# Kernel optimization log

Hardware: AMD Instinct MI355X
Metric: run time of the kernel (lower is better)

The kernel has to match this reference:

```python
import jax, jax.numpy as jnp
import numpy as np

N0, N1, N2 = 200000, 100000, 50000
D = 16          # sampled neighbor fan-out
DIM = 128       # input_dim == hidden dims


def setup_inputs() -> dict:
    key = jax.random.key(0)
    ks = jax.random.split(key, 9)
    return {
        "features": jax.random.normal(ks[0], (N0, DIM), jnp.float32),
        "W1": jax.random.normal(ks[1], (2 * DIM, DIM), jnp.float32) * 0.02,
        "b1": jnp.zeros((DIM,), jnp.float32),
        "W2": jax.random.normal(ks[2], (2 * DIM, DIM), jnp.float32) * 0.02,
        "b2": jnp.zeros((DIM,), jnp.float32),
        "neigh1_idx": jax.random.randint(ks[3], (N1, D), 0, N0, jnp.int32),
        "self1_idx": jax.random.randint(ks[4], (N1,), 0, N0, jnp.int32),
        "neigh2_idx": jax.random.randint(ks[5], (N2, D), 0, N1, jnp.int32),
        "self2_idx": jax.random.randint(ks[6], (N2,), 0, N1, jnp.int32),
    }


def _sage_layer(h_prev, self_idx, neigh_idx, W, b):
    # mean-aggregate sampled neighbors: gather [n, D, d] -> mean over D
    neigh = jnp.mean(h_prev[neigh_idx], axis=1)          # [n, d]
    x = jnp.concatenate([h_prev[self_idx], neigh], axis=-1)  # [n, 2d]
    return jax.nn.relu(x @ W + b)                        # [n, d_out]


def reference(features, W1, b1, W2, b2, neigh1_idx, self1_idx, neigh2_idx, self2_idx):
    h1 = _sage_layer(features, self1_idx, neigh1_idx, W1, b1)  # [N1, DIM]
    h2 = _sage_layer(h1, self2_idx, neigh2_idx, W2, b2)        # [N2, DIM]
    return h2
```

## Files before the change

### kernel.cpp

```cpp
#include <hip/hip_runtime.h>
#include <hip/hip_bf16.h>

typedef __attribute__((ext_vector_type(8))) short bf16x8;
typedef __attribute__((ext_vector_type(4))) float f32x4;

#define DIM   128
#define KD    256
#define FAN   16
#define TILE  32
#define XS_STRIDE 264
#define WP_LAYER_SHORTS (8*8*64*8)

__device__ __forceinline__ unsigned short f2bf(float f) {
    __hip_bfloat16 h = __float2bfloat16(f);
    return *reinterpret_cast<unsigned short*>(&h);
}
__device__ __forceinline__ float bflo(unsigned int u) { return __uint_as_float(u << 16); }
__device__ __forceinline__ float bfhi(unsigned int u) { return __uint_as_float(u & 0xffff0000u); }

__global__ __launch_bounds__(256)
void cvt_bf16_kernel(const float* __restrict__ in, uint2* __restrict__ out, int n4)
{
    const int stride = gridDim.x * blockDim.x;
    for (int i = blockIdx.x * blockDim.x + threadIdx.x; i < n4; i += stride) {
        const float4 v = reinterpret_cast<const float4*>(in)[i];
        uint2 o;
        o.x = (unsigned int)f2bf(v.x) | ((unsigned int)f2bf(v.y) << 16);
        o.y = (unsigned int)f2bf(v.z) | ((unsigned int)f2bf(v.w) << 16);
        out[i] = o;
    }
}

__global__ __launch_bounds__(256)
void wpack_kernel(const float* __restrict__ W1, const float* __restrict__ W2,
                  unsigned short* __restrict__ wp)
{
    const int b = blockIdx.x;
    const float* W = (b & 8) ? W2 : W1;
    unsigned short* dst = wp + ((b & 8) ? WP_LAYER_SHORTS : 0);
    const int t   = b & 7;
    const int tid = threadIdx.x;
    const int lane = tid & 63, wid = tid >> 6;
    const int l15 = lane & 15, lg = lane >> 4;
    #pragma unroll
    for (int s = 0; s < 2; ++s) {
        const int ks = wid + s * 4;
        bf16x8 v;
        #pragma unroll
        for (int j = 0; j < 8; ++j)
            v[j] = (short)f2bf(W[(size_t)(ks * 32 + lg * 8 + j) * DIM + t * 16 + l15]);
        *reinterpret_cast<bf16x8*>(dst + ((size_t)(t * 8 + ks) * 64 + lane) * 8) = v;
    }
}

template<bool SRC_BF, bool DST_BF>
__global__ __launch_bounds__(256, 4)
void sage_layer(const void* __restrict__ src,
                const unsigned short* __restrict__ wp,
                const float* __restrict__ bias,
                const int*  __restrict__ nidx,
                const int*  __restrict__ sidx,
                void* __restrict__ dst,
                int nnodes)
{
    __shared__ unsigned short xs[TILE * XS_STRIDE];

    const int tid  = threadIdx.x;
    const int lane = tid & 63;
    const int wid  = tid >> 6;
    const int l15  = lane & 15;
    const int lg   = lane >> 4;
    const int nb   = blockIdx.x * TILE;

    #pragma unroll 4
    for (int i = 0; i < 8; ++i) {
        int n = nb + wid * 8 + i;
        if (n >= nnodes) n = nnodes - 1;
        const int sn = sidx[n];
        const int* nn = nidx + (size_t)n * FAN;
        unsigned int su;
        float ax = 0.f, ay = 0.f;
        if (SRC_BF) {
            const unsigned int* srcu = (const unsigned int*)src;
            su = srcu[(size_t)sn * 64 + lane];
            #pragma unroll
            for (int j = 0; j < FAN; ++j) {
                const unsigned int u = srcu[(size_t)nn[j] * 64 + lane];
                ax += bflo(u); ay += bfhi(u);
            }
        } else {
            const float* srcf = (const float*)src;
            const float2 sv = *reinterpret_cast<const float2*>(srcf + (size_t)sn * DIM + 2 * lane);
            su = (unsigned int)f2bf(sv.x) | ((unsigned int)f2bf(sv.y) << 16);
            #pragma unroll
            for (int j = 0; j < FAN; ++j) {
                const float2 v = *reinterpret_cast<const float2*>(srcf + (size_t)nn[j] * DIM + 2 * lane);
                ax += v.x; ay += v.y;
            }
        }
        ax *= 0.0625f; ay *= 0.0625f;
        const unsigned int mu = (unsigned int)f2bf(ax) | ((unsigned int)f2bf(ay) << 16);
        unsigned int* row = reinterpret_cast<unsigned int*>(xs + (size_t)(wid * 8 + i) * XS_STRIDE);
        row[lane]      = su;
        row[64 + lane] = mu;
    }

    bf16x8 wf[2][8];
    #pragma unroll
    for (int t = 0; t < 2; ++t) {
        const int tg = 2 * wid + t;
        #pragma unroll
        for (int ks = 0; ks < 8; ++ks)
            wf[t][ks] = *reinterpret_cast<const bf16x8*>(
                wp + ((size_t)(tg * 8 + ks) * 64 + lane) * 8);
    }
    float bv[2];
    bv[0] = bias[(2 * wid + 0) * 16 + l15];
    bv[1] = bias[(2 * wid + 1) * 16 + l15];

    __syncthreads();

    f32x4 acc[2][2];
    #pragma unroll
    for (int mt = 0; mt < 2; ++mt)
        #pragma unroll
        for (int t = 0; t < 2; ++t)
            acc[mt][t] = (f32x4){0.f, 0.f, 0.f, 0.f};

    #pragma unroll
    for (int ks = 0; ks < 8; ++ks) {
        bf16x8 af[2];
        #pragma unroll
        for (int mt = 0; mt < 2; ++mt)
            af[mt] = *reinterpret_cast<const bf16x8*>(
                xs + (size_t)(mt * 16 + l15) * XS_STRIDE + ks * 32 + lg * 8);
        #pragma unroll
        for (int mt = 0; mt < 2; ++mt)
            #pragma unroll
            for (int t = 0; t < 2; ++t)
                acc[mt][t] = __builtin_amdgcn_mfma_f32_16x16x32_bf16(
                    af[mt], wf[t][ks], acc[mt][t], 0, 0, 0);
    }

    #pragma unroll
    for (int mt = 0; mt < 2; ++mt) {
        #pragma unroll
        for (int t = 0; t < 2; ++t) {
            const int col = (2 * wid + t) * 16 + l15;
            #pragma unroll
            for (int r = 0; r < 4; ++r) {
                const int n = nb + mt * 16 + lg * 4 + r;
                if (n < nnodes) {
                    const float v = acc[mt][t][r] + bv[t];
                    const float rv = v > 0.f ? v : 0.f;
                    if (DST_BF)
                        ((unsigned short*)dst)[(size_t)n * DIM + col] = f2bf(rv);
                    else
                        ((float*)dst)[(size_t)n * DIM + col] = rv;
                }
            }
        }
    }
}

extern "C" void kernel_launch(void* const* d_in, const int* in_sizes, int n_in,
                              void* d_out, int out_size, void* d_ws, size_t ws_size,
                              hipStream_t stream)
{
    const float* features = (const float*)d_in[0];
    const float* W1       = (const float*)d_in[1];
    const float* b1       = (const float*)d_in[2];
    const float* W2       = (const float*)d_in[3];
    const float* b2       = (const float*)d_in[4];
    const int*   n1idx    = (const int*)d_in[5];
    const int*   s1idx    = (const int*)d_in[6];
    const int*   n2idx    = (const int*)d_in[7];
    const int*   s2idx    = (const int*)d_in[8];

    const int NF = in_sizes[0];
    const int N1 = in_sizes[6];
    const int N2 = in_sizes[8];

    const size_t fbf_bytes = (size_t)NF * 2;
    const size_t h1_bytes  = (size_t)N1 * DIM * 2;
    const size_t wp_bytes  = (size_t)2 * WP_LAYER_SHORTS * 2;
    const bool full = ws_size >= fbf_bytes + h1_bytes + wp_bytes;

    unsigned char* ws = (unsigned char*)d_ws;
    unsigned short* fbf = nullptr;
    unsigned short* h1  = nullptr;
    unsigned short* wpk = nullptr;
    if (full) {
        fbf = (unsigned short*)ws;
        h1  = (unsigned short*)(ws + fbf_bytes);
        wpk = (unsigned short*)(ws + fbf_bytes + h1_bytes);
    } else {
        h1  = (unsigned short*)ws;
        wpk = (unsigned short*)(ws + h1_bytes);
    }

    wpack_kernel<<<16, 256, 0, stream>>>(W1, W2, wpk);
    if (full)
        cvt_bf16_kernel<<<2048, 256, 0, stream>>>(features, (uint2*)fbf, NF / 4);

    const int t1 = (N1 + TILE - 1) / TILE;
    const int t2 = (N2 + TILE - 1) / TILE;

    if (full)
        sage_layer<true,  true><<<t1, 256, 0, stream>>>(fbf, wpk, b1, n1idx, s1idx, h1, N1);
    else
        sage_layer<false, true><<<t1, 256, 0, stream>>>(features, wpk, b1, n1idx, s1idx, h1, N1);

    sage_layer<true, false><<<t2, 256, 0, stream>>>(h1, wpk + WP_LAYER_SHORTS, b2,
                                                    n2idx, s2idx, (float*)d_out, N2);
}
```

Before: 274.2 us.

## Restructure SAGE layer into single-wave blocks streaming weights from memory

Changes each block to one 64-lane wave handling a 16-node tile, which removes the block barrier and the register-resident weight fragments. Weights are now loaded from global memory per k-step for all 8 output column tiles, and the loop is not unrolled. The aim is lower register and LDS pressure for more resident waves to hide gather latency. The cost is that every block re-reads the full packed weight matrix, adding L2 traffic, and each wave gathers its 16 nodes serially.

```diff
diff --git a/kernel.cpp b/kernel.cpp
--- a/kernel.cpp
+++ b/kernel.cpp
@@ -7,7 +7,7 @@
 #define DIM   128
 #define KD    256
 #define FAN   16
-#define TILE  32
+#define TILE  16
 #define XS_STRIDE 264
 #define WP_LAYER_SHORTS (8*8*64*8)
 
@@ -54,7 +54,7 @@
 }
 
 template<bool SRC_BF, bool DST_BF>
-__global__ __launch_bounds__(256, 4)
+__global__ __launch_bounds__(64, 5)
 void sage_layer(const void* __restrict__ src,
                 const unsigned short* __restrict__ wp,
                 const float* __restrict__ bias,
@@ -65,16 +65,14 @@
 {
     __shared__ unsigned short xs[TILE * XS_STRIDE];
 
-    const int tid  = threadIdx.x;
-    const int lane = tid & 63;
-    const int wid  = tid >> 6;
+    const int lane = threadIdx.x;
     const int l15  = lane & 15;
     const int lg   = lane >> 4;
     const int nb   = blockIdx.x * TILE;
 
     #pragma unroll 4
-    for (int i = 0; i < 8; ++i) {
-        int n = nb + wid * 8 + i;
+    for (int i = 0; i < TILE; ++i) {
+        int n = nb + i;
         if (n >= nnodes) n = nnodes - 1;
         const int sn = sidx[n];
         const int* nn = nidx + (size_t)n * FAN;
@@ -100,64 +98,41 @@
         }
         ax *= 0.0625f; ay *= 0.0625f;
         const unsigned int mu = (unsigned int)f2bf(ax) | ((unsigned int)f2bf(ay) << 16);
-        unsigned int* row = reinterpret_cast<unsigned int*>(xs + (size_t)(wid * 8 + i) * XS_STRIDE);
+        unsigned int* row = reinterpret_cast<unsigned int*>(xs + (size_t)i * XS_STRIDE);
         row[lane]      = su;
         row[64 + lane] = mu;
     }
 
-    bf16x8 wf[2][8];
+    f32x4 acc[8];
     #pragma unroll
-    for (int t = 0; t < 2; ++t) {
-        const int tg = 2 * wid + t;
+    for (int t = 0; t < 8; ++t) acc[t] = (f32x4){0.f, 0.f, 0.f, 0.f};
+
+    #pragma unroll 1
+    for (int ks = 0; ks < 8; ++ks) {
+        const bf16x8 af = *reinterpret_cast<const bf16x8*>(
+            xs + (size_t)l15 * XS_STRIDE + ks * 32 + lg * 8);
         #pragma unroll
-        for (int ks = 0; ks < 8; ++ks)
-            wf[t][ks] = *reinterpret_cast<const bf16x8*>(
-                wp + ((size_t)(tg * 8 + ks) * 64 + lane) * 8);
-    }
-    float bv[2];
-    bv[0] = bias[(2 * wid + 0) * 16 + l15];
-    bv[1] = bias[(2 * wid + 1) * 16 + l15];
-
-    __syncthreads();
-
-    f32x4 acc[2][2];
-    #pragma unroll
-    for (int mt = 0; mt < 2; ++mt)
-        #pragma unroll
-        for (int t = 0; t < 2; ++t)
-            acc[mt][t] = (f32x4){0.f, 0.f, 0.f, 0.f};
-
-    #pragma unroll
-    for (int ks = 0; ks < 8; ++ks) {
-        bf16x8 af[2];
-        #pragma unroll
-        for (int mt = 0; mt < 2; ++mt)
-            af[mt] = *reinterpret_cast<const bf16x8*>(
-                xs + (size_t)(mt * 16 + l15) * XS_STRIDE + ks * 32 + lg * 8);
-        #pragma unroll
-        for (int mt = 0; mt < 2; ++mt)
-            #pragma unroll
-            for (int t = 0; t < 2; ++t)
-                acc[mt][t] = __builtin_amdgcn_mfma_f32_16x16x32_bf16(
-                    af[mt], wf[t][ks], acc[mt][t], 0, 0, 0);
+        for (int t = 0; t < 8; ++t) {
+            const bf16x8 w = *reinterpret_cast<const bf16x8*>(
+                wp + ((size_t)(t * 8 + ks) * 64 + lane) * 8);
+            acc[t] = __builtin_amdgcn_mfma_f32_16x16x32_bf16(af, w, acc[t], 0, 0, 0);
+        }
     }
 
     #pragma unroll
-    for (int mt = 0; mt < 2; ++mt) {
+    for (int t = 0; t < 8; ++t) {
+        const int col = t * 16 + l15;
+        const float bvt = bias[col];
         #pragma unroll
-        for (int t = 0; t < 2; ++t) {
-            const int col = (2 * wid + t) * 16 + l15;
-            #pragma unroll
-            for (int r = 0; r < 4; ++r) {
-                const int n = nb + mt * 16 + lg * 4 + r;
-                if (n < nnodes) {
-                    const float v = acc[mt][t][r] + bv[t];
-                    const float rv = v > 0.f ? v : 0.f;
-                    if (DST_BF)
-                        ((unsigned short*)dst)[(size_t)n * DIM + col] = f2bf(rv);
-                    else
-                        ((float*)dst)[(size_t)n * DIM + col] = rv;
-                }
+        for (int r = 0; r < 4; ++r) {
+            const int n = nb + lg * 4 + r;
+            if (n < nnodes) {
+                const float v = acc[t][r] + bvt;
+                const float rv = v > 0.f ? v : 0.f;
+                if (DST_BF)
+                    ((unsigned short*)dst)[(size_t)n * DIM + col] = f2bf(rv);
+                else
+                    ((float*)dst)[(size_t)n * DIM + col] = rv;
             }
         }
     }
@@ -207,10 +182,10 @@
     const int t2 = (N2 + TILE - 1) / TILE;
 
     if (full)
-        sage_layer<true,  true><<<t1, 256, 0, stream>>>(fbf, wpk, b1, n1idx, s1idx, h1, N1);
+        sage_layer<true,  true><<<t1, 64, 0, stream>>>(fbf, wpk, b1, n1idx, s1idx, h1, N1);
     else
-        sage_layer<false, true><<<t1, 256, 0, stream>>>(features, wpk, b1, n1idx, s1idx, h1, N1);
+        sage_layer<false, true><<<t1, 64, 0, stream>>>(features, wpk, b1, n1idx, s1idx, h1, N1);
 
-    sage_layer<true, false><<<t2, 256, 0, stream>>>(h1, wpk + WP_LAYER_SHORTS, b2,
-                                                    n2idx, s2idx, (float*)d_out, N2);
+    sage_layer<true, false><<<t2, 64, 0, stream>>>(h1, wpk + WP_LAYER_SHORTS, b2,
+                                                   n2idx, s2idx, (float*)d_out, N2);
 }
```

New measurement: 360.1 us. 1.31x slower.
